# Optimization experiments

Hardware: AMD Instinct MI355X
Metric: run time of the kernel (lower is better)

## Reference

```python
import jax, jax.numpy as jnp
import numpy as np

N_EMBED = 384
BLOCK_SIZE = 256
HEAD_SIZE = 64
BATCH = 1024


def setup_inputs() -> dict:
    key = jax.random.key(0)
    kx, kq, kk, kv = jax.random.split(key, 4)
    x = jax.random.normal(kx, (BATCH, BLOCK_SIZE, N_EMBED), dtype=jnp.float32)
    # nn.Linear(n_embed, head_size, bias=False) weights, stored as [in, out]
    s = 1.0 / np.sqrt(N_EMBED)
    Wq = jax.random.normal(kq, (N_EMBED, HEAD_SIZE), dtype=jnp.float32) * s
    Wk = jax.random.normal(kk, (N_EMBED, HEAD_SIZE), dtype=jnp.float32) * s
    Wv = jax.random.normal(kv, (N_EMBED, HEAD_SIZE), dtype=jnp.float32) * s
    return {"x": x, "Wq": Wq, "Wk": Wk, "Wv": Wv}


def reference(x, Wq, Wk, Wv):
    B, T, C = x.shape  # C == n_embed
    q = x @ Wq  # [B, T, H]
    k = x @ Wk  # [B, T, H]
    v = x @ Wv  # [B, T, H]
    # NOTE: original scales by C**-0.5 where C = n_embed (not head_size)
    wei = jnp.einsum('bth,bsh->bts', q, k) * (C ** -0.5)  # [B, T, T]
    causal = jnp.tril(jnp.ones((T, T), dtype=bool))
    wei = jnp.where(causal, wei, -jnp.inf)
    wei = jax.nn.softmax(wei, axis=-1)
    # dropout is identity in eval mode
    out = jnp.einsum('bts,bsh->bth', wei, v)  # [B, T, H]
    return out
```

## Files before the change

kernel.cpp:

```cpp
#include <hip/hip_runtime.h>
#include <hip/hip_bf16.h>

#define BATCH 1024
#define SEQ   256
#define CEMB  384
#define HD    64
#define LDQ   72
#define LDV   264
#define LDP   40

#define SCALE 0.051031036307982884f
#define LOG2E 1.4426950408889634f

typedef __bf16 bf16x8 __attribute__((ext_vector_type(8)));
typedef float  f32x4  __attribute__((ext_vector_type(4)));

__global__ void repack_w_kernel(const float* __restrict__ Wq,
                                const float* __restrict__ Wk,
                                const float* __restrict__ Wv,
                                __bf16* __restrict__ Wt) {
    int idx = blockIdx.x * blockDim.x + threadIdx.x;
    if (idx >= 3 * HD * CEMB) return;
    int p   = idx / (HD * CEMB);
    int rem = idx - p * (HD * CEMB);
    int n   = rem / CEMB;
    int k   = rem - n * CEMB;
    const float* W = (p == 0) ? Wq : (p == 1) ? Wk : Wv;
    Wt[idx] = (__bf16)W[k * HD + n];
}

__launch_bounds__(512, 2)
__global__ void head_kernel(const float* __restrict__ x,
                            const __bf16* __restrict__ Wt,
                            float* __restrict__ out) {
    __shared__ __align__(16) __bf16 shQ[SEQ][LDQ];
    __shared__ __align__(16) __bf16 shK[SEQ][LDQ];
    __shared__ __align__(16) __bf16 shVT[HD][LDV];
    __shared__ __align__(16) __bf16 shX[SEQ][LDQ];

    const int b    = blockIdx.x;
    const int tid  = threadIdx.x;
    const int wave = tid >> 6;
    const int lane = tid & 63;
    const int q4   = lane >> 4;
    const int l15  = lane & 15;

    const f32x4 fzero = {0.f, 0.f, 0.f, 0.f};

    f32x4 accP[3][2][4];
    #pragma unroll
    for (int p = 0; p < 3; ++p)
        #pragma unroll
        for (int mi = 0; mi < 2; ++mi)
            #pragma unroll
            for (int jn = 0; jn < 4; ++jn) accP[p][mi][jn] = fzero;

    const size_t xbase = (size_t)b * SEQ * CEMB;
    for (int kc = 0; kc < 6; ++kc) {
        #pragma unroll
        for (int pass = 0; pass < 4; ++pass) {
            int t   = pass * 64 + (tid >> 3);
            int seg = (tid & 7) * 8;
            f32x4 lo = *(const f32x4*)(x + xbase + (size_t)t * CEMB + kc * 64 + seg);
            f32x4 hi = *(const f32x4*)(x + xbase + (size_t)t * CEMB + kc * 64 + seg + 4);
            bf16x8 val;
            #pragma unroll
            for (int i = 0; i < 4; ++i) { val[i] = (__bf16)lo[i]; val[i + 4] = (__bf16)hi[i]; }
            *(bf16x8*)&shX[t][seg] = val;
        }
        __syncthreads();
        #pragma unroll
        for (int ks = 0; ks < 2; ++ks) {
            bf16x8 afrag[2];
            #pragma unroll
            for (int mi = 0; mi < 2; ++mi)
                afrag[mi] = *(const bf16x8*)&shX[wave * 32 + mi * 16 + l15][ks * 32 + q4 * 8];
            #pragma unroll
            for (int p = 0; p < 3; ++p) {
                #pragma unroll
                for (int jn = 0; jn < 4; ++jn) {
                    bf16x8 bfrag = *(const bf16x8*)(Wt + (size_t)(p * HD + jn * 16 + l15) * CEMB
                                                      + kc * 64 + ks * 32 + q4 * 8);
                    #pragma unroll
                    for (int mi = 0; mi < 2; ++mi)
                        accP[p][mi][jn] = __builtin_amdgcn_mfma_f32_16x16x32_bf16(
                            afrag[mi], bfrag, accP[p][mi][jn], 0, 0, 0);
                }
            }
        }
        __syncthreads();
    }

    #pragma unroll
    for (int mi = 0; mi < 2; ++mi)
        #pragma unroll
        for (int jn = 0; jn < 4; ++jn)
            #pragma unroll
            for (int r = 0; r < 4; ++r) {
                int t = wave * 32 + mi * 16 + q4 * 4 + r;
                int h = jn * 16 + l15;
                shQ[t][h]  = (__bf16)accP[0][mi][jn][r];
                shK[t][h]  = (__bf16)accP[1][mi][jn][r];
                shVT[h][t] = (__bf16)accP[2][mi][jn][r];
            }
    __syncthreads();

    __bf16* stg = &shX[0][0] + wave * (16 * LDP);

    #pragma unroll
    for (int m = 0; m < 2; ++m) {
        const int mt = m ? (15 - wave) : wave;

        f32x4 accS[16];
        #pragma unroll
        for (int j = 0; j < 16; ++j) accS[j] = fzero;

        bf16x8 aq[2];
        #pragma unroll
        for (int ks = 0; ks < 2; ++ks)
            aq[ks] = *(const bf16x8*)&shQ[mt * 16 + l15][ks * 32 + q4 * 8];

        #pragma unroll
        for (int j = 0; j < 16; ++j) {
            if (j <= mt) {
                bf16x8 bk0 = *(const bf16x8*)&shK[j * 16 + l15][q4 * 8];
                bf16x8 bk1 = *(const bf16x8*)&shK[j * 16 + l15][32 + q4 * 8];
                accS[j] = __builtin_amdgcn_mfma_f32_16x16x32_bf16(aq[0], bk0, accS[j], 0, 0, 0);
                accS[j] = __builtin_amdgcn_mfma_f32_16x16x32_bf16(aq[1], bk1, accS[j], 0, 0, 0);
            }
        }

        float mx[4] = {-1e30f, -1e30f, -1e30f, -1e30f};
        #pragma unroll
        for (int j = 0; j < 16; ++j) {
            if (j > mt) continue;
            #pragma unroll
            for (int r = 0; r < 4; ++r) {
                float sv = accS[j][r] * SCALE;
                bool valid = (j < mt) || (l15 <= q4 * 4 + r);
                sv = valid ? sv : -1e30f;
                accS[j][r] = sv;
                mx[r] = fmaxf(mx[r], sv);
            }
        }
        #pragma unroll
        for (int off = 1; off < 16; off <<= 1)
            #pragma unroll
            for (int r = 0; r < 4; ++r)
                mx[r] = fmaxf(mx[r], __shfl_xor(mx[r], off, 64));

        float sm[4] = {0.f, 0.f, 0.f, 0.f};
        #pragma unroll
        for (int j = 0; j < 16; ++j) {
            if (j > mt) continue;
            #pragma unroll
            for (int r = 0; r < 4; ++r) {
                float pv = exp2f((accS[j][r] - mx[r]) * LOG2E);
                accS[j][r] = pv;
                sm[r] += pv;
            }
        }
        #pragma unroll
        for (int off = 1; off < 16; off <<= 1)
            #pragma unroll
            for (int r = 0; r < 4; ++r)
                sm[r] += __shfl_xor(sm[r], off, 64);
        float rinv[4];
        #pragma unroll
        for (int r = 0; r < 4; ++r) rinv[r] = 1.0f / sm[r];

        f32x4 accO[4] = {fzero, fzero, fzero, fzero};
        const int ksmax = (mt * 16 + 15) >> 5;
        #pragma unroll
        for (int ks = 0; ks < 8; ++ks) {
            if (ks > ksmax) continue;
            __asm__ __volatile__("" ::: "memory");
            #pragma unroll
            for (int jj = 0; jj < 2; ++jj) {
                int j = 2 * ks + jj;
                #pragma unroll
                for (int r = 0; r < 4; ++r) {
                    float pv = (j <= mt) ? (float)accS[j][r] : 0.0f;
                    stg[(q4 * 4 + r) * LDP + jj * 16 + l15] = (__bf16)pv;
                }
            }
            __asm__ __volatile__("s_waitcnt lgkmcnt(0)" ::: "memory");
            bf16x8 ap = *(const bf16x8*)(stg + l15 * LDP + q4 * 8);
            #pragma unroll
            for (int hj = 0; hj < 4; ++hj) {
                bf16x8 bv = *(const bf16x8*)&shVT[hj * 16 + l15][ks * 32 + q4 * 8];
                accO[hj] = __builtin_amdgcn_mfma_f32_16x16x32_bf16(ap, bv, accO[hj], 0, 0, 0);
            }
        }

        #pragma unroll
        for (int hj = 0; hj < 4; ++hj)
            #pragma unroll
            for (int r = 0; r < 4; ++r) {
                int t = mt * 16 + q4 * 4 + r;
                int h = hj * 16 + l15;
                out[((size_t)b * SEQ + t) * HD + h] = accO[hj][r] * rinv[r];
            }
    }
}

extern "C" void kernel_launch(void* const* d_in, const int* in_sizes, int n_in,
                              void* d_out, int out_size, void* d_ws, size_t ws_size,
                              hipStream_t stream) {
    const float* x  = (const float*)d_in[0];
    const float* Wq = (const float*)d_in[1];
    const float* Wk = (const float*)d_in[2];
    const float* Wv = (const float*)d_in[3];
    __bf16* Wt = (__bf16*)d_ws;
    float* out = (float*)d_out;

    repack_w_kernel<<<(3 * HD * CEMB + 255) / 256, 256, 0, stream>>>(Wq, Wk, Wv, Wt);
    head_kernel<<<BATCH, 512, 0, stream>>>(x, Wt, out);
}
```

Measured before the change: 661.6 us.

## Load x directly into MFMA fragments and keep Q in registers

Each wave now computes projections for exactly the two query tiles it later handles (wave and 15-wave), loading x straight from global memory into bf16 A-fragments instead of staging it through shared memory with barriers. Q stays in registers and is re-laid-out through a small per-wave staging buffer, which removes the shQ and shX arrays and cuts LDS use enough to raise the launch-bounds occupancy target to 4 blocks. s_setprio is wrapped around the MFMA loops. The trade-off is uncoalesced global x loads (a row stride per lane) and possibly more register pressure under the higher occupancy target.

```diff
diff --git a/kernel.cpp b/kernel.cpp
--- a/kernel.cpp
+++ b/kernel.cpp
@@ -5,7 +5,7 @@
 #define SEQ   256
 #define CEMB  384
 #define HD    64
-#define LDQ   72
+#define LDK   72
 #define LDV   264
 #define LDP   40
 
@@ -29,14 +29,13 @@
     Wt[idx] = (__bf16)W[k * HD + n];
 }
 
-__launch_bounds__(512, 2)
+__launch_bounds__(512, 4)
 __global__ void head_kernel(const float* __restrict__ x,
                             const __bf16* __restrict__ Wt,
                             float* __restrict__ out) {
-    __shared__ __align__(16) __bf16 shQ[SEQ][LDQ];
-    __shared__ __align__(16) __bf16 shK[SEQ][LDQ];
+    __shared__ __align__(16) __bf16 shK[SEQ][LDK];
     __shared__ __align__(16) __bf16 shVT[HD][LDV];
-    __shared__ __align__(16) __bf16 shX[SEQ][LDQ];
+    __shared__ __align__(16) __bf16 stg8[8][16 * LDP];
 
     const int b    = blockIdx.x;
     const int tid  = threadIdx.x;
@@ -47,6 +46,9 @@
 
     const f32x4 fzero = {0.f, 0.f, 0.f, 0.f};
 
+    const int trow0 = wave * 16;
+    const int trow1 = (15 - wave) * 16;
+
     f32x4 accP[3][2][4];
     #pragma unroll
     for (int p = 0; p < 3; ++p)
@@ -56,70 +58,79 @@
             for (int jn = 0; jn < 4; ++jn) accP[p][mi][jn] = fzero;
 
     const size_t xbase = (size_t)b * SEQ * CEMB;
+    const float* xr0 = x + xbase + (size_t)(trow0 + l15) * CEMB + q4 * 8;
+    const float* xr1 = x + xbase + (size_t)(trow1 + l15) * CEMB + q4 * 8;
+
+    #pragma unroll
     for (int kc = 0; kc < 6; ++kc) {
         #pragma unroll
-        for (int pass = 0; pass < 4; ++pass) {
-            int t   = pass * 64 + (tid >> 3);
-            int seg = (tid & 7) * 8;
-            f32x4 lo = *(const f32x4*)(x + xbase + (size_t)t * CEMB + kc * 64 + seg);
-            f32x4 hi = *(const f32x4*)(x + xbase + (size_t)t * CEMB + kc * 64 + seg + 4);
-            bf16x8 val;
-            #pragma unroll
-            for (int i = 0; i < 4; ++i) { val[i] = (__bf16)lo[i]; val[i + 4] = (__bf16)hi[i]; }
-            *(bf16x8*)&shX[t][seg] = val;
-        }
-        __syncthreads();
-        #pragma unroll
         for (int ks = 0; ks < 2; ++ks) {
-            bf16x8 afrag[2];
-            #pragma unroll
-            for (int mi = 0; mi < 2; ++mi)
-                afrag[mi] = *(const bf16x8*)&shX[wave * 32 + mi * 16 + l15][ks * 32 + q4 * 8];
+            const int koff = kc * 64 + ks * 32;
+            f32x4 lo0 = *(const f32x4*)(xr0 + koff);
+            f32x4 hi0 = *(const f32x4*)(xr0 + koff + 4);
+            f32x4 lo1 = *(const f32x4*)(xr1 + koff);
+            f32x4 hi1 = *(const f32x4*)(xr1 + koff + 4);
+            bf16x8 af0, af1;
+            #pragma unroll
+            for (int i = 0; i < 4; ++i) {
+                af0[i] = (__bf16)lo0[i]; af0[i + 4] = (__bf16)hi0[i];
+                af1[i] = (__bf16)lo1[i]; af1[i + 4] = (__bf16)hi1[i];
+            }
             #pragma unroll
             for (int p = 0; p < 3; ++p) {
                 #pragma unroll
                 for (int jn = 0; jn < 4; ++jn) {
                     bf16x8 bfrag = *(const bf16x8*)(Wt + (size_t)(p * HD + jn * 16 + l15) * CEMB
-                                                      + kc * 64 + ks * 32 + q4 * 8);
-                    #pragma unroll
-                    for (int mi = 0; mi < 2; ++mi)
-                        accP[p][mi][jn] = __builtin_amdgcn_mfma_f32_16x16x32_bf16(
-                            afrag[mi], bfrag, accP[p][mi][jn], 0, 0, 0);
+                                                      + koff + q4 * 8);
+                    accP[p][0][jn] = __builtin_amdgcn_mfma_f32_16x16x32_bf16(
+                        af0, bfrag, accP[p][0][jn], 0, 0, 0);
+                    accP[p][1][jn] = __builtin_amdgcn_mfma_f32_16x16x32_bf16(
+                        af1, bfrag, accP[p][1][jn], 0, 0, 0);
                 }
             }
         }
-        __syncthreads();
     }
 
     #pragma unroll
-    for (int mi = 0; mi < 2; ++mi)
+    for (int mi = 0; mi < 2; ++mi) {
+        const int trow = mi ? trow1 : trow0;
         #pragma unroll
         for (int jn = 0; jn < 4; ++jn)
             #pragma unroll
             for (int r = 0; r < 4; ++r) {
-                int t = wave * 32 + mi * 16 + q4 * 4 + r;
+                int t = trow + q4 * 4 + r;
                 int h = jn * 16 + l15;
-                shQ[t][h]  = (__bf16)accP[0][mi][jn][r];
                 shK[t][h]  = (__bf16)accP[1][mi][jn][r];
                 shVT[h][t] = (__bf16)accP[2][mi][jn][r];
             }
+    }
     __syncthreads();
 
-    __bf16* stg = &shX[0][0] + wave * (16 * LDP);
+    __bf16* stg = &stg8[wave][0];
 
     #pragma unroll
     for (int m = 0; m < 2; ++m) {
         const int mt = m ? (15 - wave) : wave;
 
+        bf16x8 aq[2];
+        #pragma unroll
+        for (int hf = 0; hf < 2; ++hf) {
+            #pragma unroll
+            for (int jj = 0; jj < 2; ++jj) {
+                const int jn = hf * 2 + jj;
+                #pragma unroll
+                for (int r = 0; r < 4; ++r)
+                    stg[(q4 * 4 + r) * LDP + jj * 16 + l15] = (__bf16)accP[0][m][jn][r];
+            }
+            __asm__ __volatile__("s_waitcnt lgkmcnt(0)" ::: "memory");
+            aq[hf] = *(const bf16x8*)(stg + l15 * LDP + q4 * 8);
+        }
+
         f32x4 accS[16];
         #pragma unroll
         for (int j = 0; j < 16; ++j) accS[j] = fzero;
 
-        bf16x8 aq[2];
-        #pragma unroll
-        for (int ks = 0; ks < 2; ++ks)
-            aq[ks] = *(const bf16x8*)&shQ[mt * 16 + l15][ks * 32 + q4 * 8];
-
+        __builtin_amdgcn_s_setprio(1);
         #pragma unroll
         for (int j = 0; j < 16; ++j) {
             if (j <= mt) {
@@ -129,6 +140,7 @@
                 accS[j] = __builtin_amdgcn_mfma_f32_16x16x32_bf16(aq[1], bk1, accS[j], 0, 0, 0);
             }
         }
+        __builtin_amdgcn_s_setprio(0);
 
         float mx[4] = {-1e30f, -1e30f, -1e30f, -1e30f};
         #pragma unroll
@@ -186,11 +198,13 @@
             }
             __asm__ __volatile__("s_waitcnt lgkmcnt(0)" ::: "memory");
             bf16x8 ap = *(const bf16x8*)(stg + l15 * LDP + q4 * 8);
+            __builtin_amdgcn_s_setprio(1);
             #pragma unroll
             for (int hj = 0; hj < 4; ++hj) {
                 bf16x8 bv = *(const bf16x8*)&shVT[hj * 16 + l15][ks * 32 + q4 * 8];
                 accO[hj] = __builtin_amdgcn_mfma_f32_16x16x32_bf16(ap, bv, accO[hj], 0, 0, 0);
             }
+            __builtin_amdgcn_s_setprio(0);
         }
 
         #pragma unroll
```

New measurement: 874.5 us. 32.2% more time.
